# Performance work log

Measured on AMD Instinct MI355X. Metric: run time of the kernel, lower is better.

## Reference

```python
import jax, jax.numpy as jnp
import numpy as np

N = 100000
E = 1600000
D = 64

def setup_inputs() -> dict:
    key = jax.random.key(0)
    k1, k2, k3, k4, k5, k6 = jax.random.split(key, 6)
    h = jax.random.normal(k1, (N, D), dtype=jnp.float32)
    w = jax.random.uniform(k2, (E, 1), dtype=jnp.float32)
    src = jax.random.randint(k3, (E,), 0, N, dtype=jnp.int32)
    dst = jax.random.randint(k4, (E,), 0, N, dtype=jnp.int32)
    W = jax.random.normal(k5, (D, 2 * D), dtype=jnp.float32) / np.sqrt(2 * D)
    b = jax.random.normal(k6, (D,), dtype=jnp.float32) * 0.01
    return {"h": h, "w": w, "src": src, "dst": dst, "W": W, "b": b}

def reference(h, w, src, dst, W, b):
    # messages: per-edge weight times gathered source features  [E, D]
    m = w * h[src]
    # scatter-sum into destination nodes  [N, D]
    agg = jax.ops.segment_sum(m, dst, num_segments=N)
    # concat self + aggregated, then linear: [N, 2D] @ [2D, D] + b
    return jnp.concatenate([h, agg], axis=1) @ W.T + b
```

## Files before the change

### kernel.cpp

```cpp
#include <hip/hip_runtime.h>

#define D 64
#define CAP 32
#define WQ_BITS 15
#define WQ_MAX 32767.0f
#define NSHARDS 8

typedef int   int4v   __attribute__((ext_vector_type(4)));
typedef float float4v __attribute__((ext_vector_type(4)));

__device__ __forceinline__ ushort f2bf(float x) {
    unsigned u = __float_as_uint(x);
    unsigned r = (u + 0x7fff + ((u >> 16) & 1)) >> 16;
    return (ushort)r;
}
__device__ __forceinline__ float bf2f(ushort u) {
    return __uint_as_float(((unsigned)u) << 16);
}

__global__ __launch_bounds__(256) void scatter_shard_kernel(
    const int* __restrict__ src, const int* __restrict__ dst,
    const float* __restrict__ w, int* __restrict__ cursor,
    unsigned* __restrict__ ovBits, unsigned* __restrict__ pairs,
    int E, int N)
{
    int shard   = blockIdx.x & (NSHARDS - 1);
    int slice   = blockIdx.x >> 3;
    int nSlices = gridDim.x >> 3;
    int n8 = (N + NSHARDS - 1) / NSHARDS;
    int lo = shard * n8;
    int hi = min(N, lo + n8);

    int e4 = E >> 2;
    for (int gi = slice * 256 + threadIdx.x; gi < e4; gi += nSlices * 256) {
        int e0 = gi * 4;
        int4v d4 = *(const int4v*)&dst[e0];
        #pragma unroll
        for (int i = 0; i < 4; ++i) {
            int d = d4[i];
            if (d >= lo && d < hi) {
                int e = e0 + i;
                int sv = __builtin_nontemporal_load(&src[e]);
                float wvr = __builtin_nontemporal_load(&w[e]);
                int pos = atomicAdd(&cursor[d], 1);
                if (pos < CAP) {
                    float wv = fminf(fmaxf(wvr, 0.f), 1.f);
                    unsigned wq = (unsigned)(wv * WQ_MAX + 0.5f);
                    pairs[(size_t)d * CAP + pos] =
                        ((unsigned)sv << WQ_BITS) | wq;
                } else {
                    atomicOr(&ovBits[e >> 5], 1u << (e & 31));
                }
            }
        }
    }
    for (int e = e4 * 4 + slice * 256 + threadIdx.x; e < E; e += nSlices * 256) {
        int d = dst[e];
        if (d >= lo && d < hi) {
            int pos = atomicAdd(&cursor[d], 1);
            if (pos < CAP) {
                float wv = fminf(fmaxf(w[e], 0.f), 1.f);
                unsigned wq = (unsigned)(wv * WQ_MAX + 0.5f);
                pairs[(size_t)d * CAP + pos] =
                    ((unsigned)src[e] << WQ_BITS) | wq;
            } else {
                atomicOr(&ovBits[e >> 5], 1u << (e & 31));
            }
        }
    }
}

__global__ __launch_bounds__(256) void gemm_fused_kernel(
    const float* __restrict__ h, const float* __restrict__ W,
    const float* __restrict__ b, float* __restrict__ out,
    ushort* __restrict__ g, int N)
{
    __shared__ float Wt[128 * 64];
    __shared__ float Xt[64 * 64];
    int tid = threadIdx.x;

    for (int idx = tid; idx < 128 * 64; idx += 256) {
        int j = idx & 63;
        int k = idx >> 6;
        Wt[k * 64 + j] = W[j * 128 + k];
    }

    int n0blk = blockIdx.x * 64;
    {
        int n = tid & 63;
        int krow = tid >> 6;
        int nn = min(n0blk + n, N - 1);
        #pragma unroll
        for (int c = 0; c < 4; ++c) {
            int k0 = (krow + c * 4) * 4;
            float4 v = *(const float4*)&h[(size_t)nn * D + k0];
            Xt[(k0 + 0) * 64 + n] = v.x;
            Xt[(k0 + 1) * 64 + n] = v.y;
            Xt[(k0 + 2) * 64 + n] = v.z;
            Xt[(k0 + 3) * 64 + n] = v.w;
        }
    }
    __syncthreads();

    int j0 = (tid & 15) * 4;
    int nb = (tid >> 4) * 4;

    float4 bv = *(const float4*)&b[j0];
    float accS[4][4], accG[4][4];
    #pragma unroll
    for (int i = 0; i < 4; ++i) {
        accS[i][0] = bv.x; accS[i][1] = bv.y; accS[i][2] = bv.z; accS[i][3] = bv.w;
        accG[i][0] = 0.f;  accG[i][1] = 0.f;  accG[i][2] = 0.f;  accG[i][3] = 0.f;
    }

    #pragma unroll 4
    for (int k = 0; k < 64; ++k) {
        float4 xv = *(const float4*)&Xt[k * 64 + nb];
        float4 w1 = *(const float4*)&Wt[k * 64 + j0];
        float4 w2 = *(const float4*)&Wt[(k + 64) * 64 + j0];
        #pragma unroll
        for (int i = 0; i < 4; ++i) {
            float x = (&xv.x)[i];
            accS[i][0] += x * w1.x; accS[i][1] += x * w1.y;
            accS[i][2] += x * w1.z; accS[i][3] += x * w1.w;
            accG[i][0] += x * w2.x; accG[i][1] += x * w2.y;
            accG[i][2] += x * w2.z; accG[i][3] += x * w2.w;
        }
    }

    #pragma unroll
    for (int i = 0; i < 4; ++i) {
        int n = n0blk + nb + i;
        if (n < N) {
            *(float4*)&out[(size_t)n * D + j0] =
                make_float4(accS[i][0], accS[i][1], accS[i][2], accS[i][3]);
            ushort4 gv;
            gv.x = f2bf(accG[i][0]); gv.y = f2bf(accG[i][1]);
            gv.z = f2bf(accG[i][2]); gv.w = f2bf(accG[i][3]);
            *(ushort4*)&g[(size_t)n * D + j0] = gv;
        }
    }
}

__global__ __launch_bounds__(256) void final_agg_kernel(
    const ushort* __restrict__ g, const unsigned* __restrict__ pairs,
    const int* __restrict__ cursor, float* __restrict__ out, int N)
{
    int wave = threadIdx.x >> 6;
    int lane = threadIdx.x & 63;
    int n = blockIdx.x * 4 + wave;
    if (n >= N) return;
    int cnt = min(cursor[n], CAP);
    unsigned mycode = (lane < CAP) ? pairs[(size_t)n * CAP + lane] : 0u;
    float acc = out[(size_t)n * D + lane];

    const float wscale = 1.0f / WQ_MAX;
    int j = 0;
    for (; j + 16 <= cnt; j += 16) {
        unsigned c[16];
        float v[16];
        #pragma unroll
        for (int u = 0; u < 16; ++u) c[u] = __shfl(mycode, j + u);
        #pragma unroll
        for (int u = 0; u < 16; ++u)
            v[u] = bf2f(g[(size_t)(c[u] >> WQ_BITS) * D + lane]);
        #pragma unroll
        for (int u = 0; u < 16; ++u)
            acc += (float)(c[u] & 0x7fffu) * wscale * v[u];
    }
    for (; j + 4 <= cnt; j += 4) {
        unsigned c[4];
        float v[4];
        #pragma unroll
        for (int u = 0; u < 4; ++u) c[u] = __shfl(mycode, j + u);
        #pragma unroll
        for (int u = 0; u < 4; ++u)
            v[u] = bf2f(g[(size_t)(c[u] >> WQ_BITS) * D + lane]);
        #pragma unroll
        for (int u = 0; u < 4; ++u)
            acc += (float)(c[u] & 0x7fffu) * wscale * v[u];
    }
    for (; j < cnt; ++j) {
        unsigned c = __shfl(mycode, j);
        acc += (float)(c & 0x7fffu) * wscale *
               bf2f(g[(size_t)(c >> WQ_BITS) * D + lane]);
    }
    out[(size_t)n * D + lane] = acc;
}

__global__ __launch_bounds__(256) void overflow_kernel(
    const unsigned* __restrict__ ovBits, const int* __restrict__ src,
    const int* __restrict__ dst, const float* __restrict__ w,
    const ushort* __restrict__ g, float* __restrict__ out, int numWords)
{
    int idx = blockIdx.x * 256 + threadIdx.x;
    for (int wi = idx; wi < numWords; wi += gridDim.x * 256) {
        unsigned bits = ovBits[wi];
        while (bits) {
            int bit = __ffs(bits) - 1;
            bits &= bits - 1;
            int e = wi * 32 + bit;
            int s = src[e], d = dst[e];
            float wv = w[e];
            for (int f = 0; f < D; ++f)
                atomicAdd(&out[(size_t)d * D + f], wv * bf2f(g[(size_t)s * D + f]));
        }
    }
}

__global__ __launch_bounds__(256) void edge_scatter_kernel(
    const float* __restrict__ h, const float* __restrict__ w,
    const int* __restrict__ src, const int* __restrict__ dst,
    float* __restrict__ agg, int E)
{
    int e = blockIdx.x * 4 + (threadIdx.x >> 6);
    int lane = threadIdx.x & 63;
    if (e >= E) return;
    float val = w[e] * h[(size_t)src[e] * D + lane];
    atomicAdd(&agg[(size_t)dst[e] * D + lane], val);
}

__global__ __launch_bounds__(256) void out_linear_kernel(
    const float* __restrict__ h, const float* __restrict__ agg,
    const float* __restrict__ W, const float* __restrict__ b,
    float* __restrict__ out, int N)
{
    __shared__ float Wt[128 * 64];
    int lane = threadIdx.x & 63;
    int waveInBlock = threadIdx.x >> 6;
    int wavesPerBlock = blockDim.x >> 6;
    for (int idx = threadIdx.x; idx < 128 * 64; idx += blockDim.x) {
        int j = idx & 63;
        int k = idx >> 6;
        Wt[k * 64 + j] = W[j * 128 + k];
    }
    __syncthreads();
    float bj = b[lane];
    int wavesPerGrid = gridDim.x * wavesPerBlock;
    for (int n = blockIdx.x * wavesPerBlock + waveInBlock; n < N; n += wavesPerGrid) {
        float hreg = h[(size_t)n * D + lane];
        float areg = agg[(size_t)n * D + lane];
        float acc = bj;
        #pragma unroll
        for (int k = 0; k < 64; ++k) {
            float hk = __shfl(hreg, k, 64);
            float ak = __shfl(areg, k, 64);
            acc += hk * Wt[k * 64 + lane];
            acc += ak * Wt[(k + 64) * 64 + lane];
        }
        out[(size_t)n * D + lane] = acc;
    }
}

extern "C" void kernel_launch(void* const* d_in, const int* in_sizes, int n_in,
                              void* d_out, int out_size, void* d_ws, size_t ws_size,
                              hipStream_t stream) {
    const float* h   = (const float*)d_in[0];
    const float* w   = (const float*)d_in[1];
    const int*   src = (const int*)d_in[2];
    const int*   dst = (const int*)d_in[3];
    const float* W   = (const float*)d_in[4];
    const float* b   = (const float*)d_in[5];
    float* out = (float*)d_out;

    int N = in_sizes[0] / D;
    int E = in_sizes[1];
    int numWords = (E + 31) / 32;

    auto align256 = [](size_t x) { return (x + 255) & ~(size_t)255; };
    size_t cursorB = align256((size_t)N * 4);
    size_t ovB     = align256((size_t)numWords * 4);
    size_t pairsB  = align256((size_t)N * CAP * 4);
    size_t gB      = align256((size_t)N * D * 2);
    size_t need = cursorB + ovB + pairsB + gB;

    if (ws_size >= need && N <= (1 << 17)) {
        char* p = (char*)d_ws;
        int*      cursor = (int*)p;       p += cursorB;
        unsigned* ovBits = (unsigned*)p;  p += ovB;
        unsigned* pairs  = (unsigned*)p;  p += pairsB;
        ushort*   g      = (ushort*)p;

        hipMemsetAsync(cursor, 0, cursorB + ovB, stream);

        scatter_shard_kernel<<<4096, 256, 0, stream>>>(src, dst, w, cursor,
                                                       ovBits, pairs, E, N);
        gemm_fused_kernel<<<(N + 63) / 64, 256, 0, stream>>>(h, W, b, out, g, N);
        final_agg_kernel<<<(N + 3) / 4, 256, 0, stream>>>(g, pairs, cursor, out, N);
        overflow_kernel<<<64, 256, 0, stream>>>(ovBits, src, dst, w, g, out, numWords);
    } else {
        float* agg = out;
        hipMemsetAsync(agg, 0, (size_t)N * D * 4, stream);
        edge_scatter_kernel<<<(E + 3) / 4, 256, 0, stream>>>(h, w, src, dst, agg, E);
        out_linear_kernel<<<2048, 256, 0, stream>>>(h, agg, W, b, out, N);
    }
}
```

Measured before the change: 259.2 us.

## Merge scatter and GEMM into one launch with bf16 weights in LDS

Combines the edge-scatter kernel and the node GEMM kernel into a single launch: the first blocks bucket edges and the rest compute the GEMM tiles, so the two independent phases can run at the same time on the GPU. The W tile is stored in LDS as bf16 to cut shared memory from 48KB to 32KB, which allows more resident blocks, and dst is now read with nontemporal loads. In exchange, every block reserves 32KB of LDS, which limits how many scatter blocks can be resident, and the self and aggregate weights lose precision.

```diff
diff --git a/kernel.cpp b/kernel.cpp
--- a/kernel.cpp
+++ b/kernel.cpp
@@ -5,6 +5,7 @@
 #define WQ_BITS 15
 #define WQ_MAX 32767.0f
 #define NSHARDS 8
+#define SCAT_BLOCKS 4096
 
 typedef int   int4v   __attribute__((ext_vector_type(4)));
 typedef float float4v __attribute__((ext_vector_type(4)));
@@ -18,74 +19,76 @@
     return __uint_as_float(((unsigned)u) << 16);
 }
 
-__global__ __launch_bounds__(256) void scatter_shard_kernel(
+__global__ __launch_bounds__(256) void fused_scatter_gemm_kernel(
     const int* __restrict__ src, const int* __restrict__ dst,
     const float* __restrict__ w, int* __restrict__ cursor,
     unsigned* __restrict__ ovBits, unsigned* __restrict__ pairs,
-    int E, int N)
-{
-    int shard   = blockIdx.x & (NSHARDS - 1);
-    int slice   = blockIdx.x >> 3;
-    int nSlices = gridDim.x >> 3;
-    int n8 = (N + NSHARDS - 1) / NSHARDS;
-    int lo = shard * n8;
-    int hi = min(N, lo + n8);
-
-    int e4 = E >> 2;
-    for (int gi = slice * 256 + threadIdx.x; gi < e4; gi += nSlices * 256) {
-        int e0 = gi * 4;
-        int4v d4 = *(const int4v*)&dst[e0];
-        #pragma unroll
-        for (int i = 0; i < 4; ++i) {
-            int d = d4[i];
+    const float* __restrict__ h, const float* __restrict__ W,
+    const float* __restrict__ b, float* __restrict__ out,
+    ushort* __restrict__ g, int E, int N)
+{
+    __shared__ char ldsRaw[32 * 1024];
+
+    if (blockIdx.x < SCAT_BLOCKS) {
+        int shard   = blockIdx.x & (NSHARDS - 1);
+        int slice   = blockIdx.x >> 3;
+        int nSlices = SCAT_BLOCKS >> 3;
+        int n8 = (N + NSHARDS - 1) / NSHARDS;
+        int lo = shard * n8;
+        int hi = min(N, lo + n8);
+
+        int e4 = E >> 2;
+        for (int gi = slice * 256 + threadIdx.x; gi < e4; gi += nSlices * 256) {
+            int e0 = gi * 4;
+            int4v d4 = __builtin_nontemporal_load((const int4v*)&dst[e0]);
+            #pragma unroll
+            for (int i = 0; i < 4; ++i) {
+                int d = d4[i];
+                if (d >= lo && d < hi) {
+                    int e = e0 + i;
+                    int sv = __builtin_nontemporal_load(&src[e]);
+                    float wvr = __builtin_nontemporal_load(&w[e]);
+                    int pos = atomicAdd(&cursor[d], 1);
+                    if (pos < CAP) {
+                        float wv = fminf(fmaxf(wvr, 0.f), 1.f);
+                        unsigned wq = (unsigned)(wv * WQ_MAX + 0.5f);
+                        pairs[(size_t)d * CAP + pos] =
+                            ((unsigned)sv << WQ_BITS) | wq;
+                    } else {
+                        atomicOr(&ovBits[e >> 5], 1u << (e & 31));
+                    }
+                }
+            }
+        }
+        for (int e = e4 * 4 + slice * 256 + threadIdx.x; e < E; e += nSlices * 256) {
+            int d = dst[e];
             if (d >= lo && d < hi) {
-                int e = e0 + i;
-                int sv = __builtin_nontemporal_load(&src[e]);
-                float wvr = __builtin_nontemporal_load(&w[e]);
                 int pos = atomicAdd(&cursor[d], 1);
                 if (pos < CAP) {
-                    float wv = fminf(fmaxf(wvr, 0.f), 1.f);
+                    float wv = fminf(fmaxf(w[e], 0.f), 1.f);
                     unsigned wq = (unsigned)(wv * WQ_MAX + 0.5f);
                     pairs[(size_t)d * CAP + pos] =
-                        ((unsigned)sv << WQ_BITS) | wq;
+                        ((unsigned)src[e] << WQ_BITS) | wq;
                 } else {
                     atomicOr(&ovBits[e >> 5], 1u << (e & 31));
                 }
             }
         }
-    }
-    for (int e = e4 * 4 + slice * 256 + threadIdx.x; e < E; e += nSlices * 256) {
-        int d = dst[e];
-        if (d >= lo && d < hi) {
-            int pos = atomicAdd(&cursor[d], 1);
-            if (pos < CAP) {
-                float wv = fminf(fmaxf(w[e], 0.f), 1.f);
-                unsigned wq = (unsigned)(wv * WQ_MAX + 0.5f);
-                pairs[(size_t)d * CAP + pos] =
-                    ((unsigned)src[e] << WQ_BITS) | wq;
-            } else {
-                atomicOr(&ovBits[e >> 5], 1u << (e & 31));
-            }
-        }
-    }
-}
-
-__global__ __launch_bounds__(256) void gemm_fused_kernel(
-    const float* __restrict__ h, const float* __restrict__ W,
-    const float* __restrict__ b, float* __restrict__ out,
-    ushort* __restrict__ g, int N)
-{
-    __shared__ float Wt[128 * 64];
-    __shared__ float Xt[64 * 64];
+        return;
+    }
+
+    ushort* Wt = (ushort*)ldsRaw;
+    float*  Xt = (float*)(ldsRaw + 16384);
     int tid = threadIdx.x;
+    int tile = blockIdx.x - SCAT_BLOCKS;
 
     for (int idx = tid; idx < 128 * 64; idx += 256) {
         int j = idx & 63;
         int k = idx >> 6;
-        Wt[k * 64 + j] = W[j * 128 + k];
-    }
-
-    int n0blk = blockIdx.x * 64;
+        Wt[k * 64 + j] = f2bf(W[j * 128 + k]);
+    }
+
+    int n0blk = tile * 64;
     {
         int n = tid & 63;
         int krow = tid >> 6;
@@ -116,15 +119,17 @@
     #pragma unroll 4
     for (int k = 0; k < 64; ++k) {
         float4 xv = *(const float4*)&Xt[k * 64 + nb];
-        float4 w1 = *(const float4*)&Wt[k * 64 + j0];
-        float4 w2 = *(const float4*)&Wt[(k + 64) * 64 + j0];
+        ushort4 w1h = *(const ushort4*)&Wt[k * 64 + j0];
+        ushort4 w2h = *(const ushort4*)&Wt[(k + 64) * 64 + j0];
+        float w10 = bf2f(w1h.x), w11 = bf2f(w1h.y), w12 = bf2f(w1h.z), w13 = bf2f(w1h.w);
+        float w20 = bf2f(w2h.x), w21 = bf2f(w2h.y), w22 = bf2f(w2h.z), w23 = bf2f(w2h.w);
         #pragma unroll
         for (int i = 0; i < 4; ++i) {
             float x = (&xv.x)[i];
-            accS[i][0] += x * w1.x; accS[i][1] += x * w1.y;
-            accS[i][2] += x * w1.z; accS[i][3] += x * w1.w;
-            accG[i][0] += x * w2.x; accG[i][1] += x * w2.y;
-            accG[i][2] += x * w2.z; accG[i][3] += x * w2.w;
+            accS[i][0] += x * w10; accS[i][1] += x * w11;
+            accS[i][2] += x * w12; accS[i][3] += x * w13;
+            accG[i][0] += x * w20; accG[i][1] += x * w21;
+            accG[i][2] += x * w22; accG[i][3] += x * w23;
         }
     }
 
@@ -283,9 +288,9 @@
 
         hipMemsetAsync(cursor, 0, cursorB + ovB, stream);
 
-        scatter_shard_kernel<<<4096, 256, 0, stream>>>(src, dst, w, cursor,
-                                                       ovBits, pairs, E, N);
-        gemm_fused_kernel<<<(N + 63) / 64, 256, 0, stream>>>(h, W, b, out, g, N);
+        int gemmTiles = (N + 63) / 64;
+        fused_scatter_gemm_kernel<<<SCAT_BLOCKS + gemmTiles, 256, 0, stream>>>(
+            src, dst, w, cursor, ovBits, pairs, h, W, b, out, g, E, N);
         final_agg_kernel<<<(N + 3) / 4, 256, 0, stream>>>(g, pairs, cursor, out, N);
         overflow_kernel<<<64, 256, 0, stream>>>(ovBits, src, dst, w, g, out, numWords);
     } else {
```

Result: no change. 263.5 us (+1.7%).
